# Kernel tuning notes

Hardware: AMD Instinct MI355X
Metric: run time of the kernel (lower is better)

Reference implementation:

```python
import math
import jax, jax.numpy as jnp
import numpy as np

IMG = 1024.0
B = 16
# (h, w, stride, anchor_size) per FPN level
LEVELS = [(256, 256, 4, 32), (128, 128, 8, 64), (64, 64, 16, 128), (32, 32, 32, 256), (16, 16, 64, 512)]
A = 3  # anchors per location (ratios 0.5, 1, 2)
PRE_NMS = 1000   # per level
POST_NMS = 1000
NMS_THRES = 0.7
MIN_SIZE = 1.0
NEG = -1e9
BBOX_CLIP = math.log(1000.0 / 16.0)  # torchvision BoxCoder clamp


def _make_anchors():
    ratios = np.array([0.5, 1.0, 2.0], np.float32)
    hr = np.sqrt(ratios)
    wr = 1.0 / hr
    out = []
    for (h, w, stride, size) in LEVELS:
        ws, hs = size * wr, size * hr
        base = np.stack([-ws / 2, -hs / 2, ws / 2, hs / 2], axis=1)  # [A,4]
        sx = np.arange(w, dtype=np.float32) * stride
        sy = np.arange(h, dtype=np.float32) * stride
        gy, gx = np.meshgrid(sy, sx, indexing='ij')
        shifts = np.stack([gx.ravel(), gy.ravel(), gx.ravel(), gy.ravel()], axis=1)  # [h*w,4]
        out.append((shifts[:, None, :] + base[None, :, :]).reshape(-1, 4))
    return np.concatenate(out, axis=0).astype(np.float32)  # [261888,4]


def setup_inputs() -> dict:
    key = jax.random.key(0)
    ks = jax.random.split(key, 10)
    inp = {}
    for i, (h, w, _, _) in enumerate(LEVELS):
        inp[f'cls{i}'] = jax.random.normal(ks[i], (B, A, h, w), jnp.float32)
        inp[f'box{i}'] = jax.random.normal(ks[5 + i], (B, 4 * A, h, w), jnp.float32) * 0.1
    inp['anchors'] = jnp.asarray(_make_anchors())
    return inp


def _process(x, C):
    # view(B,-1,C,h,w) -> permute(0,3,4,1,2) -> reshape(B,-1,C)
    b, ac, h, w = x.shape
    a = ac // C
    return x.reshape(b, a, C, h, w).transpose(0, 3, 4, 1, 2).reshape(b, -1, C)


def _decode(deltas, anchors):
    # BoxCoder.decode with weights (1,1,1,1)
    aw = anchors[..., 2] - anchors[..., 0]
    ah = anchors[..., 3] - anchors[..., 1]
    ax = anchors[..., 0] + 0.5 * aw
    ay = anchors[..., 1] + 0.5 * ah
    dx, dy = deltas[..., 0], deltas[..., 1]
    dw = jnp.minimum(deltas[..., 2], BBOX_CLIP)
    dh = jnp.minimum(deltas[..., 3], BBOX_CLIP)
    px = dx * aw + ax
    py = dy * ah + ay
    pw = jnp.exp(dw) * aw
    ph = jnp.exp(dh) * ah
    return jnp.stack([px - 0.5 * pw, py - 0.5 * ph, px + 0.5 * pw, py + 0.5 * ph], axis=-1)


def _iou_one_vs_all(box, boxes):
    lt = jnp.maximum(box[:2], boxes[:, :2])
    rb = jnp.minimum(box[2:], boxes[:, 2:])
    wh = jnp.clip(rb - lt, 0.0)
    inter = wh[:, 0] * wh[:, 1]
    a1 = (box[2] - box[0]) * (box[3] - box[1])
    a2 = (boxes[:, 2] - boxes[:, 0]) * (boxes[:, 3] - boxes[:, 1])
    return inter / (a1 + a2 - inter + 1e-9)


def _nms(boxes, scores):
    # iterative hard NMS, fixed POST_NMS iterations (jit-friendly)
    def step(sc, _):
        j = jnp.argmax(sc)
        s = sc[j]
        b = boxes[j]
        valid = s > NEG * 0.5
        iou = _iou_one_vs_all(b, boxes)
        sc = jnp.where(iou > NMS_THRES, NEG, sc)
        sc = sc.at[j].set(NEG)
        return sc, (jnp.where(valid, b, 0.0), jnp.where(valid, s, NEG))
    _, (kb, ks) = jax.lax.scan(step, scores, None, length=POST_NMS)
    return kb, ks


def _forward(clsL, boxL, anchors):
    obj = jnp.concatenate([_process(c, 1) for c in clsL], axis=1)[..., 0]   # [B, N]
    deltas = jnp.concatenate([_process(b, 4) for b in boxL], axis=1)        # [B, N, 4]
    proposals = _decode(jax.lax.stop_gradient(deltas), anchors[None])       # [B, N, 4]

    # per-level pre-NMS top-k on objectness logits
    idx_list, off = [], 0
    for (h, w, _, _) in LEVELS:
        n_l = A * h * w
        k = min(PRE_NMS, n_l)
        _, idx = jax.lax.top_k(obj[:, off:off + n_l], k)
        idx_list.append(idx + off)
        off += n_l
    idx = jnp.concatenate(idx_list, axis=1)                                 # [B, K]

    logits = jnp.take_along_axis(obj, idx, axis=1)
    boxes = jnp.take_along_axis(proposals, idx[..., None], axis=1)
    boxes = jnp.clip(boxes, 0.0, IMG)                                       # clip to image
    probs = jax.nn.sigmoid(logits)
    ws = boxes[..., 2] - boxes[..., 0]
    hs = boxes[..., 3] - boxes[..., 1]
    keep = (ws >= MIN_SIZE) & (hs >= MIN_SIZE)                              # remove small boxes
    probs = jnp.where(keep, probs, NEG)

    kb, ks = jax.vmap(_nms)(boxes, probs)                                   # [B,POST_NMS,4],[B,POST_NMS]
    return kb, ks


def reference(cls0, cls1, cls2, cls3, cls4, box0, box1, box2, box3, box4, anchors):
    return _forward([cls0, cls1, cls2, cls3, cls4], [box0, box1, box2, box3, box4], anchors)
```

## Files before the change

kernel.cpp:

```cpp
#include <hip/hip_runtime.h>
#include <stdint.h>


#define NBATCH 16
#define KSUM 4768
#define NEGF -1e9f
#define CAP 4096
#define CAPB 4096
#define PFX 1664
#define PW 26
typedef unsigned long long u64;
typedef unsigned int u32;

struct Ptrs {
  const float* cls[5];
  const float* box[5];
  const float* anc;
};

__constant__ int c_hw[5]      = {65536, 16384, 4096, 1024, 256};
__constant__ int c_lghw[5]    = {16, 14, 12, 10, 8};
__constant__ int c_K[5]       = {1000, 1000, 1000, 1000, 768};
__constant__ int c_levNOff[5] = {0, 196608, 245760, 258048, 261120};
__constant__ int c_selOff[5]  = {0, 1000, 2000, 3000, 4000};
__constant__ u32 c_guess[4] = {0xC0133333u, 0xBFE00000u, 0xBF8CCCCDu, 0xBE4CCCCDu};

__device__ __forceinline__ u32 monokey(float f) {
  u32 u = __float_as_uint(f);
  return (u & 0x80000000u) ? ~u : (u | 0x80000000u);
}
__device__ __forceinline__ float inv_monokey(u32 k) {
  return __uint_as_float((k & 0x80000000u) ? (k ^ 0x80000000u) : ~k);
}
__device__ __forceinline__ u64 lanemask_lt(int lane) {
  return lane ? ((~0ULL) >> (64 - lane)) : 0ULL;
}

__device__ float sigmoid_xla(float x) {
  #pragma clang fp contract(off)
  float h = 0.5f * x;
  float hc = fminf(fmaxf(h, -7.90531110763549805f), 7.90531110763549805f);
  float x2 = hc * hc;
  float p = -2.76076847742355e-16f;
  p = p * x2 + 2.00018790482477e-13f;
  p = p * x2 + -8.60467152213735e-11f;
  p = p * x2 + 5.12229709037114e-08f;
  p = p * x2 + 1.48572235717979e-05f;
  p = p * x2 + 6.37261928875436e-04f;
  p = p * x2 + 4.89352455891786e-03f;
  p = hc * p;
  float q = 1.19825839466702e-06f;
  q = q * x2 + 1.18534705686654e-04f;
  q = q * x2 + 2.26843463243900e-03f;
  q = q * x2 + 4.89352518554385e-03f;
  float t = (fabsf(h) < 0.0004f) ? h : (p / q);
  return 0.5f + 0.5f * t;
}

__device__ void decode_box(float4 anc, float dx, float dy, float dw, float dh,
                           float& x0, float& y0, float& x1, float& y1, bool& keep) {
  #pragma clang fp contract(off)
  float aw = anc.z - anc.x;
  float ah = anc.w - anc.y;
  float ax = anc.x + 0.5f * aw;
  float ay = anc.y + 0.5f * ah;
  float dwc = fminf(dw, 4.135166556742356f);
  float dhc = fminf(dh, 4.135166556742356f);
  float px = dx * aw + ax;
  float py = dy * ah + ay;
  float pw = expf(dwc) * aw;
  float ph = expf(dhc) * ah;
  x0 = px - 0.5f * pw;
  y0 = py - 0.5f * ph;
  x1 = px + 0.5f * pw;
  y1 = py + 0.5f * ph;
  x0 = fminf(fmaxf(x0, 0.0f), 1024.0f);
  y0 = fminf(fmaxf(y0, 0.0f), 1024.0f);
  x1 = fminf(fmaxf(x1, 0.0f), 1024.0f);
  y1 = fminf(fmaxf(y1, 0.0f), 1024.0f);
  keep = ((x1 - x0) >= 1.0f) && ((y1 - y0) >= 1.0f);
}

__device__ __forceinline__ bool iou_gt(float4 a, float aa, float4 b, float ba) {
  #pragma clang fp contract(off)
  float w = fmaxf(fminf(a.z, b.z) - fmaxf(a.x, b.x), 0.0f);
  float h = fmaxf(fminf(a.w, b.w) - fmaxf(a.y, b.y), 0.0f);
  float inter = w * h;
  float denom = aa + ba - inter + 1e-9f;
  if (inter <= 0.65f * denom) return false;
  return (inter / denom) > 0.7f;
}

__device__ __forceinline__ bool pair_supp(float4 a, float aa, float4 b2, float ba) {
  #pragma clang fp contract(off)
  float w = fmaxf(fminf(a.z, b2.z) - fmaxf(a.x, b2.x), 0.0f);
  float h = fmaxf(fminf(a.w, b2.w) - fmaxf(a.y, b2.y), 0.0f);
  float inter = w * h;
  float denom = aa + ba - inter + 1e-9f;
  bool p65 = inter > 0.65f * denom;
  bool p75 = inter >= 0.75f * denom;
  bool band = p65 && !p75;
  bool supp = p75;
  if (__ballot(band) != 0ULL) {
    if (band) supp = (inter / denom) > 0.7f;
  }
  return supp;
}

__global__ __launch_bounds__(1024) void k_capture(Ptrs p, u64* __restrict__ gCand,
                                                  u32* __restrict__ gCntBlk) {
  const int blk = (int)blockIdx.x;
  const int b = blk / 12, sub = blk % 12;
  int l, s, S;
  if (sub < 8)       { l = 0; s = sub;     S = 8; }
  else if (sub < 10) { l = 1; s = sub - 8; S = 2; }
  else if (sub == 10){ l = 2; s = 0;       S = 1; }
  else               { l = 3; s = 0;       S = 1; }
  const int hw = c_hw[l], lghw = c_lghw[l];
  const int n4 = (3 * hw) >> 2;
  const int per = n4 / S;
  const int tid = threadIdx.x, lane = tid & 63;
  const float4* base4 = (const float4*)(p.cls[l] + (size_t)b * (size_t)(3 * hw)) + (size_t)s * per;
  const int pe0 = 4 * s * per;
  const u32 gk = c_guess[l];

  __shared__ __align__(16) u64 lc[CAPB];
  __shared__ u32 lcnt;
  if (tid == 0) lcnt = 0u;
  __syncthreads();

  for (int i = tid; i < per; i += 1024) {
    float4 v = base4[i];
    float fv[4] = {v.x, v.y, v.z, v.w};
    #pragma unroll
    for (int c = 0; c < 4; ++c) {
      u32 mk = monokey(fv[c]);
      bool cc = (mk >= gk);
      u64 cb = __ballot(cc);
      if (cb) {
        if (cc) {
          int pe = pe0 + 4 * i + c;
          int a = pe >> lghw, cell = pe & (hw - 1);
          u32 nloc = (u32)(cell * 3 + a);
          int leader = __builtin_ctzll(cb);
          u32 wcnt = (u32)__popcll(cb);
          u32 bs;
          if (lane == leader) bs = atomicAdd(&lcnt, wcnt);
          bs = __shfl(bs, leader);
          u32 u = bs + (u32)__popcll(cb & lanemask_lt(lane));
          if (u < CAPB) lc[u] = (((u64)mk) << 32) | nloc;
        }
      }
    }
  }
  __syncthreads();
  const u32 cnt = lcnt;
  const u32 wn = cnt < CAPB ? cnt : CAPB;
  u64* myCand = gCand + (size_t)blk * CAPB;
  for (u32 i = tid; i < wn; i += 1024) myCand[i] = lc[i];
  if (tid == 0) gCntBlk[blk] = cnt;
}

__device__ __forceinline__ void find_thresh(const u32* histF, int nb, u32 K,
                                            u32 cAbove, u32* wsum, u32* wsuf,
                                            u32* shOut, int tid) {
  const int lane = tid & 63, w = tid >> 6;
  u32 h0, h1;
  if (nb == 2048) {
    int b0 = 2 * tid, b1 = b0 + 1;
    h0 = histF[b0] + histF[2048 + b0];
    h1 = histF[b1] + histF[2048 + b1];
  } else {
    h0 = histF[tid] + histF[2048 + tid];
    h1 = 0u;
  }
  u32 x = h0 + h1;
  #pragma unroll
  for (int off = 1; off < 64; off <<= 1) {
    u32 v = __shfl_down(x, off);
    if (lane + off < 64) x += v;
  }
  if (lane == 0) wsum[w] = x;
  __syncthreads();
  if (tid == 0) {
    u32 acc = 0;
    wsuf[16] = 0u;
    for (int q = 15; q >= 0; --q) { acc += wsum[q]; wsuf[q] = acc; }
  }
  __syncthreads();
  u32 SUF0 = x + wsuf[w + 1];
  if (cAbove + SUF0 >= K && cAbove + SUF0 - h0 < K) {
    shOut[0] = (nb == 2048) ? (u32)(2 * tid) : (u32)tid;
    shOut[1] = cAbove + SUF0 - h0;
  }
  if (nb == 2048) {
    u32 SUF1 = SUF0 - h0;
    if (cAbove + SUF1 >= K && cAbove + SUF1 - h1 < K) {
      shOut[0] = (u32)(2 * tid + 1);
      shOut[1] = cAbove + SUF1 - h1;
    }
  }
  __syncthreads();
}

__global__ __launch_bounds__(1024) void k_sel2(Ptrs p, const u64* __restrict__ gCand,
                                               const u32* __restrict__ gCntBlk,
                                               u64* __restrict__ keysC,
                                               u32* __restrict__ cntOut,
                                               float4* __restrict__ boxesWs) {
  const int l = (int)(blockIdx.x % 5);
  const int b = (int)(blockIdx.x / 5);
  const int hw = c_hw[l], lghw = c_lghw[l];
  const int n = 3 * hw, K = c_K[l];
  const int tid = threadIdx.x, lane = tid & 63;

  __shared__ u32 histF[4096];
  __shared__ __align__(16) u64 slots[1024];
  __shared__ __align__(16) u64 cand[CAP];
  __shared__ u32 tieN[1024];
  __shared__ u32 sh[4];
  __shared__ u32 wsum[16], wsuf[17];
  __shared__ u32 subc[8], suboff[9], subBad;

  slots[tid] = 0ULL;
  u32* hc = &histF[((tid >> 6) & 1) * 2048];

  if (K >= n) {
    const float* base = p.cls[l] + (size_t)b * (size_t)n;
    if (tid < n) {
      u32 mk = monokey(base[tid]);
      int a = tid >> lghw, cell = tid & (hw - 1);
      u32 nloc = (u32)(cell * 3 + a);
      slots[tid] = (((u64)mk) << 32) | (0xFFFFFFFFu - nloc);
    }
    __syncthreads();
  } else {
    int subbase, S;
    if (l == 0)      { subbase = 0;  S = 8; }
    else if (l == 1) { subbase = 8;  S = 2; }
    else if (l == 2) { subbase = 10; S = 1; }
    else             { subbase = 11; S = 1; }
    if (tid < (u32)S) subc[tid] = gCntBlk[b * 12 + subbase + tid];
    __syncthreads();
    if (tid == 0) {
      u32 acc = 0, bad = 0;
      for (int t = 0; t < S; ++t) {
        suboff[t] = acc;
        if (subc[t] > CAPB) bad = 1u;
        acc += subc[t];
      }
      suboff[S] = acc;
      subBad = bad;
    }
    __syncthreads();
    const u32 nC = suboff[S];
    u32 threshKey;
    if (!subBad && nC >= (u32)K && nC <= CAP) {
      for (int t = 0; t < S; ++t) {
        const u64* src = gCand + (size_t)(b * 12 + subbase + t) * CAPB;
        u32 c0 = suboff[t], cN = subc[t];
        for (u32 i = tid; i < cN; i += 1024) cand[c0 + i] = src[i];
      }
      for (int i = tid; i < 4096; i += 1024) histF[i] = 0u;
      __syncthreads();
      for (int i = tid; i < (int)nC; i += 1024)
        atomicAdd(&hc[(u32)(cand[i] >> 32) >> 21], 1u);
      __syncthreads();
      find_thresh(histF, 2048, (u32)K, 0u, wsum, wsuf, sh, tid);
      const u32 b0 = sh[0];
      const u32 cA0 = sh[1];
      __syncthreads();
      for (int i = tid; i < 4096; i += 1024) histF[i] = 0u;
      __syncthreads();
      for (int i = tid; i < (int)nC; i += 1024) {
        u32 mk = (u32)(cand[i] >> 32);
        if ((mk >> 21) == b0) atomicAdd(&hc[(mk >> 10) & 0x7FFu], 1u);
      }
      __syncthreads();
      find_thresh(histF, 2048, (u32)K, cA0, wsum, wsuf, sh, tid);
      const u32 b1 = sh[0];
      const u32 cA1 = sh[1];
      const u32 prefix22 = (b0 << 11) | b1;
      __syncthreads();
      for (int i = tid; i < 4096; i += 1024) histF[i] = 0u;
      __syncthreads();
      for (int i = tid; i < (int)nC; i += 1024) {
        u32 mk = (u32)(cand[i] >> 32);
        if ((mk >> 10) == prefix22) atomicAdd(&hc[mk & 0x3FFu], 1u);
      }
      __syncthreads();
      find_thresh(histF, 1024, (u32)K, cA1, wsum, wsuf, sh, tid);
      threshKey = (prefix22 << 10) | sh[0];
      if (tid == 0) { sh[2] = 0u; sh[3] = 0u; }
      __syncthreads();
      for (int i = tid; i < (int)nC; i += 1024) {
        u64 e = cand[i];
        u32 mk = (u32)(e >> 32);
        u32 nloc = (u32)(e & 0xFFFFFFFFull);
        bool gt = (mk > threshKey);
        u64 gb = __ballot(gt);
        if (gt) {
          int leader = __builtin_ctzll(gb);
          u32 wcnt = (u32)__popcll(gb);
          u32 bs;
          if (lane == leader) bs = atomicAdd(&sh[2], wcnt);
          bs = __shfl(bs, leader);
          u32 s2 = bs + (u32)__popcll(gb & lanemask_lt(lane));
          slots[s2] = (((u64)mk) << 32) | (0xFFFFFFFFu - nloc);
        } else if (mk == threshKey) {
          u32 tt = atomicAdd(&sh[3], 1u);
          if (tt < 1024u) tieN[tt] = nloc;
        }
      }
      __syncthreads();
    } else {
      const float* base = p.cls[l] + (size_t)b * (size_t)n;
      const float4* base4 = (const float4*)base;
      const int n4 = n >> 2;
      u32 prefix = 0, cAbove = 0;
      for (int pass = 0; pass < 3; ++pass) {
        for (int i = tid; i < 4096; i += 1024) histF[i] = 0u;
        __syncthreads();
        for (int i = tid; i < n4; i += 1024) {
          float4 v = base4[i];
          float fv[4] = {v.x, v.y, v.z, v.w};
          #pragma unroll
          for (int c = 0; c < 4; ++c) {
            u32 mk = monokey(fv[c]);
            if (pass == 0) atomicAdd(&hc[mk >> 21], 1u);
            else if (pass == 1) { if ((mk >> 21) == prefix) atomicAdd(&hc[(mk >> 10) & 0x7FFu], 1u); }
            else { if ((mk >> 10) == prefix) atomicAdd(&hc[mk & 0x3FFu], 1u); }
          }
        }
        __syncthreads();
        find_thresh(histF, (pass == 2) ? 1024 : 2048, (u32)K, cAbove, wsum, wsuf, sh, tid);
        u32 t = sh[0];
        cAbove = sh[1];
        prefix = (pass == 0) ? t : ((prefix << ((pass == 2) ? 10 : 11)) | t);
        __syncthreads();
      }
      threshKey = prefix;
      if (tid == 0) { sh[2] = 0u; sh[3] = 0u; }
      __syncthreads();
      for (int i = tid; i < n4; i += 1024) {
        float4 v = base4[i];
        float fv[4] = {v.x, v.y, v.z, v.w};
        #pragma unroll
        for (int c = 0; c < 4; ++c) {
          u32 mk = monokey(fv[c]);
          if (mk >= threshKey) {
            int pe = 4 * i + c;
            int a = pe >> lghw, cell = pe & (hw - 1);
            u32 nloc = (u32)(cell * 3 + a);
            if (mk > threshKey) {
              u32 s2 = atomicAdd(&sh[2], 1u);
              slots[s2] = (((u64)mk) << 32) | (0xFFFFFFFFu - nloc);
            } else {
              u32 tt = atomicAdd(&sh[3], 1u);
              if (tt < 1024u) tieN[tt] = nloc;
            }
          }
        }
      }
      __syncthreads();
    }
    if (tid == 0) {
      int cnt = (int)sh[2];
      int need = K - cnt;
      int tc = (int)sh[3];
      if (tc > 1024) tc = 1024;
      for (int s2 = 0; s2 < need; ++s2) {
        u32 best = 0xFFFFFFFFu;
        int bj = -1;
        for (int i2 = 0; i2 < tc; ++i2) {
          u32 v = tieN[i2];
          if (v < best) { best = v; bj = i2; }
        }
        if (bj < 0) break;
        tieN[bj] = 0xFFFFFFFFu;
        slots[cnt + s2] = (((u64)threshKey) << 32) | (0xFFFFFFFFu - best);
      }
    }
    __syncthreads();
  }

  u64 v = slots[tid];
  for (int kk = 2; kk <= 1024; kk <<= 1) {
    for (int j = kk >> 1; j > 0; j >>= 1) {
      u64 pv;
      if (j >= 64) {
        __syncthreads();
        slots[tid] = v;
        __syncthreads();
        pv = slots[tid ^ j];
      } else {
        pv = __shfl_xor(v, j);
      }
      bool takeMax = (((tid & kk) == 0) == ((tid & j) == 0));
      v = takeMax ? ((pv > v) ? pv : v) : ((pv < v) ? pv : v);
    }
  }

  const float4* anc4 = (const float4*)p.anc;
  const float* bxbase = p.box[l];
  const int levN = c_levNOff[l], selO = c_selOff[l];
  bool keepf = false;
  u64 outKey = 0ULL;
  if (tid < K && v != 0ULL) {
    u32 mk = (u32)(v >> 32);
    u32 nloc = 0xFFFFFFFFu - (u32)(v & 0xFFFFFFFFull);
    float logit = inv_monokey(mk);
    int cell = (int)(nloc / 3u);
    int a = (int)(nloc - 3u * (u32)cell);
    const float* dptr = bxbase + (((size_t)(b * 12 + a * 4)) << lghw) + (size_t)cell;
    float dx = dptr[0];
    float dy = dptr[(size_t)hw];
    float dw = dptr[(size_t)2 * (size_t)hw];
    float dh = dptr[(size_t)3 * (size_t)hw];
    float4 anc = anc4[levN + (int)nloc];
    float x0, y0, x1, y1;
    bool keep;
    decode_box(anc, dx, dy, dw, dh, x0, y0, x1, y1, keep);
    int pos = selO + tid;
    boxesWs[(size_t)b * KSUM + (size_t)pos] = make_float4(x0, y0, x1, y1);
    if (keep) {
      float prob = sigmoid_xla(logit);
      keepf = true;
      outKey = (((u64)__float_as_uint(prob)) << 32) | (0xFFFFFFFFu - (u32)pos);
    }
  }
  u64 bal = __ballot(keepf);
  if (lane == 0) wsum[tid >> 6] = (u32)__popcll(bal);
  __syncthreads();
  if (tid < 16) {
    u32 xx = wsum[tid], orig = xx;
    #pragma unroll
    for (int off = 1; off < 16; off <<= 1) {
      u32 vv = __shfl_up(xx, off);
      if (tid >= off) xx += vv;
    }
    wsuf[tid] = xx - orig;
    if (tid == 15) cntOut[b * 5 + l] = xx;
  }
  __syncthreads();
  if (keepf) {
    u32 cidx = wsuf[tid >> 6] + (u32)__popcll(bal & lanemask_lt(lane));
    keysC[((size_t)(b * 5 + l)) * 1000 + cidx] = outKey;
  }
}

__global__ __launch_bounds__(1024) void k_merge(u64* __restrict__ keysC,
                                                const u32* __restrict__ cnt,
                                                float4* __restrict__ boxesWs,
                                                u32* __restrict__ nOut) {
  const int b = blockIdx.x;
  const int tid = threadIdx.x;
  __shared__ u64 keys[5000];
  __shared__ __align__(16) float4 boxes[KSUM];
  __shared__ u32 scnt[5];
  if (tid < 5) scnt[tid] = cnt[b * 5 + tid];
  __syncthreads();
  const int N = (int)(scnt[0] + scnt[1] + scnt[2] + scnt[3] + scnt[4]);
  for (int i = tid; i < 5000; i += 1024) {
    int l = i / 1000, ii = i - l * 1000;
    keys[i] = (ii < (int)scnt[l]) ? keysC[((size_t)(b * 5 + l)) * 1000 + ii] : 0ULL;
  }
  for (int i = tid; i < KSUM; i += 1024) boxes[i] = boxesWs[(size_t)b * KSUM + i];
  __syncthreads();
  #pragma unroll
  for (int q = 0; q < 5; ++q) {
    int s = tid + q * 1024;
    if (s < 5000) {
      int l = s / 1000, ii = s - l * 1000;
      if (ii < (int)scnt[l]) {
        u64 e = keys[s];
        int rank = ii;
        #pragma unroll
        for (int l2 = 0; l2 < 5; ++l2) {
          if (l2 == l) continue;
          int base2 = l2 * 1000;
          int lo = 0, hi = (int)scnt[l2];
          while (lo < hi) {
            int mid = (lo + hi) >> 1;
            if (keys[base2 + mid] > e) lo = mid + 1; else hi = mid;
          }
          rank += lo;
        }
        u32 pos = 0xFFFFFFFFu - (u32)(e & 0xFFFFFFFFull);
        keysC[(size_t)b * 5000 + rank] = e;
        boxesWs[(size_t)b * KSUM + rank] = boxes[pos];
      }
    }
  }
  if (tid == 0) nOut[b] = (u32)N;
}

__global__ __launch_bounds__(1024) void k_mask(const float4* __restrict__ boxesWs,
                                               const u32* __restrict__ nOut,
                                               u64* __restrict__ mat) {
  const int blk = (int)blockIdx.x;
  const int b = blk / 169;
  const int rc = blk - b * 169;
  const int ts = rc / 13, tt = rc - ts * 13;
  const int tid = threadIdx.x;
  u64* matB = mat + (size_t)b * (PW * PFX);
  const int src0 = ts << 7, tgt0 = tt << 7;
  if (ts > tt) {
    if (tid < 256) {
      int s2 = tid & 127, wsel = tid >> 7;
      matB[(size_t)(2 * tt + wsel) * PFX + (size_t)(src0 + s2)] = 0ULL;
    }
    return;
  }
  const int N = (int)nOut[b];
  const int P1 = N < PFX ? N : PFX;
  const float4* mb = boxesWs + (size_t)b * KSUM;

  __shared__ __align__(16) float4 bxS[128];
  __shared__ __align__(16) float4 bxT[128];
  __shared__ float arS[128], arT[128];
  __shared__ u64 slab[256];

  if (tid < 128) {
    int i = src0 + tid;
    float4 v = (i < P1) ? mb[i] : make_float4(0.f, 0.f, 0.f, 0.f);
    bxS[tid] = v;
    {
      #pragma clang fp contract(off)
      arS[tid] = (v.z - v.x) * (v.w - v.y);
    }
  } else if (tid < 256) {
    int j = tgt0 + (tid - 128);
    float4 v = (j < P1) ? mb[j] : make_float4(0.f, 0.f, 0.f, 0.f);
    bxT[tid - 128] = v;
    {
      #pragma clang fp contract(off)
      arT[tid - 128] = (v.z - v.x) * (v.w - v.y);
    }
  }
  __syncthreads();

  const int s = tid >> 3;
  const int slc = tid & 7;
  const float4 my = bxS[s];
  const float myA = arS[s];
  const bool diag = (ts == tt);
  u64 p0 = 0ULL, p1 = 0ULL;
  #pragma unroll
  for (int k = 0; k < 8; ++k) {
    int t = slc + (k << 3);
    bool sp = pair_supp(my, myA, bxT[t], arT[t]);
    sp = sp && (!diag || (s < t));
    p0 |= ((u64)(sp ? 1u : 0u)) << t;
  }
  #pragma unroll
  for (int k = 8; k < 16; ++k) {
    int t = slc + (k << 3);
    bool sp = pair_supp(my, myA, bxT[t], arT[t]);
    sp = sp && (!diag || (s < t));
    p1 |= ((u64)(sp ? 1u : 0u)) << (t - 64);
  }
  #pragma unroll
  for (int off = 1; off < 8; off <<= 1) {
    p0 |= __shfl_xor(p0, off);
    p1 |= __shfl_xor(p1, off);
  }
  if (slc == 0) { slab[s * 2] = p0; slab[s * 2 + 1] = p1; }
  __syncthreads();
  if (tid < 256) {
    int s2 = tid & 127, wsel = tid >> 7;
    matB[(size_t)(2 * tt + wsel) * PFX + (size_t)(src0 + s2)] = slab[s2 * 2 + wsel];
  }
}

__global__ __launch_bounds__(1024) void k_nms(const u64* __restrict__ keysC,
                                              const float4* __restrict__ boxesWs,
                                              const u32* __restrict__ nOut,
                                              const u64* __restrict__ mat,
                                              float* __restrict__ out) {
  const int b = blockIdx.x;
  const int tid = threadIdx.x;
  __shared__ u64 Uw[PW], Kw[PW], remK[PW], ukS[PW], supA[PW], newKw[PW];
  __shared__ u32 wbase[PW + 1];
  __shared__ int mS, doneS;
  __shared__ __align__(16) float4 keptBox[1000];
  __shared__ float keptArea[1000];
  __shared__ __align__(16) float4 chunkBox[128];
  __shared__ float chunkArea[128];
  __shared__ float chunkProb[128];
  __shared__ u32 chunkAlive[128];
  __shared__ u64 suppBy[256];
  __shared__ u64 sAB[2];

  const int N = (int)nOut[b];
  const int P1 = N < PFX ? N : PFX;
  const u64* mk = keysC + (size_t)b * 5000;
  const float4* mb = boxesWs + (size_t)b * KSUM;
  const u64* matC = mat + (size_t)b * (PW * PFX);

  if (tid < PW) {
    int lo = tid << 6;
    int nn = P1 - lo;
    Uw[tid] = (nn >= 64) ? ~0ULL : (nn > 0 ? ((1ULL << nn) - 1ULL) : 0ULL);
    Kw[tid] = 0ULL;
    remK[tid] = 0ULL;
  }
  __syncthreads();

  const int w = tid >> 5;
  const int sub = tid & 31;
  const u64* col = (w < PW) ? (matC + (size_t)w * PFX) : matC;

  for (int round = 0; round < PFX; ++round) {
    if (tid < PW) ukS[tid] = Uw[tid] | Kw[tid];
    __syncthreads();
    {
      u64 acc = 0ULL;
      if (w < PW) {
        int j0 = sub * 52;
        #pragma unroll 4
        for (int jj = 0; jj < 52; ++jj) {
          int j = j0 + jj;
          u64 g = ukS[j >> 6];
          u64 val = col[j];
          acc |= (((g >> (j & 63)) & 1ULL) ? val : 0ULL);
        }
        #pragma unroll
        for (int off = 16; off; off >>= 1) acc |= __shfl_xor(acc, off);
        if (sub == 0) supA[w] = acc;
      }
    }
    __syncthreads();
    if (tid < PW) newKw[tid] = Uw[tid] & ~supA[tid];
    __syncthreads();
    {
      u64 acc = 0ULL;
      if (w < PW) {
        int j0 = sub * 52;
        #pragma unroll 4
        for (int jj = 0; jj < 52; ++jj) {
          int j = j0 + jj;
          u64 g = newKw[j >> 6];
          u64 val = col[j];
          acc |= (((g >> (j & 63)) & 1ULL) ? val : 0ULL);
        }
        #pragma unroll
        for (int off = 16; off; off >>= 1) acc |= __shfl_xor(acc, off);
        if (sub == 0) remK[w] |= acc;
      }
    }
    __syncthreads();
    if (tid < PW) {
      u64 u = Uw[tid], nk = newKw[tid];
      u64 nr = (u & ~nk) & remK[tid];
      Uw[tid] = u & ~nk & ~nr;
      Kw[tid] |= nk;
    }
    __syncthreads();
    if (tid == 0) {
      int d = 1;
      for (int w2 = 0; w2 < PW; ++w2)
        if (Uw[w2]) { d = 0; break; }
      doneS = d;
    }
    __syncthreads();
    if (doneS) break;
  }

  if (tid == 0) {
    u32 acc = 0;
    for (int w2 = 0; w2 < PW; ++w2) {
      wbase[w2] = acc;
      acc += (u32)__popcll(Kw[w2]);
    }
    wbase[PW] = acc;
    mS = (acc < 1000u) ? (int)acc : 1000;
  }
  __syncthreads();
  int m = mS;

  for (int idx = tid; idx < P1; idx += 1024) {
    u64 kw = Kw[idx >> 6];
    int bit = idx & 63;
    if ((kw >> bit) & 1ULL) {
      int g = (int)wbase[idx >> 6] + __popcll(kw & ((1ULL << bit) - 1ULL));
      if (g < 1000) {
        float4 bxv = mb[idx];
        float pr = __uint_as_float((u32)(mk[idx] >> 32));
        float arv;
        {
          #pragma clang fp contract(off)
          arv = (bxv.z - bxv.x) * (bxv.w - bxv.y);
        }
        keptBox[g] = bxv;
        keptArea[g] = arv;
        ((float4*)out)[b * 1000 + g] = bxv;
        out[64000 + b * 1000 + g] = pr;
      }
    }
  }
  __syncthreads();

  for (int cs = PFX; cs < N && m < 1000; cs += 128) {
    if (tid < 128) {
      int idx = cs + tid;
      float4 bxv = make_float4(0.f, 0.f, 0.f, 0.f);
      float arv = 0.f, pr = 0.f;
      u32 alive = 0u;
      if (idx < N) {
        bxv = mb[idx];
        pr = __uint_as_float((u32)(mk[idx] >> 32));
        {
          #pragma clang fp contract(off)
          arv = (bxv.z - bxv.x) * (bxv.w - bxv.y);
        }
        alive = 1u;
      }
      chunkBox[tid] = bxv;
      chunkArea[tid] = arv;
      chunkProb[tid] = pr;
      chunkAlive[tid] = alive;
    }
    if (tid >= 128 && tid < 384) suppBy[tid - 128] = 0ULL;
    __syncthreads();

    {
      int i0 = tid & 127, sl = tid >> 7;
      float4 my = chunkBox[i0];
      float myA = chunkArea[i0];
      bool supp = false;
      #pragma unroll 4
      for (int i = sl; i < m; i += 8) {
        float ka = keptArea[i];
        float4 kb = keptBox[i];
        if (fminf(ka, myA) > 0.699f * fmaxf(ka, myA))
          supp = supp | iou_gt(kb, ka, my, myA);
      }
      if (supp) chunkAlive[i0] = 0u;
    }
    for (int pI = tid; pI < 16384; pI += 1024) {
      int i = pI >> 7, j = pI & 127;
      if (j < i) {
        float aj = chunkArea[j], ai = chunkArea[i];
        if (fminf(aj, ai) > 0.699f * fmaxf(aj, ai)) {
          if (iou_gt(chunkBox[j], aj, chunkBox[i], ai))
            atomicOr(&suppBy[i * 2 + (j >> 6)], 1ULL << (j & 63));
        }
      }
    }
    __syncthreads();

    if (tid < 64) {
      bool aliveLo = chunkAlive[tid] != 0u;
      bool aliveHi = chunkAlive[64 + tid] != 0u;
      u64 sLL = suppBy[tid * 2];
      u64 sHL = suppBy[(64 + tid) * 2];
      u64 sHH = suppBy[(64 + tid) * 2 + 1];
      u64 uLo = sLL;
      #pragma unroll
      for (int off = 1; off < 64; off <<= 1) uLo |= __shfl_xor(uLo, off);
      u64 rem = uLo;
      while (rem) {
        int k = __builtin_ctzll(rem);
        rem &= rem - 1ULL;
        u64 A = __ballot(aliveLo);
        if (((A >> k) & 1ULL) && ((sLL >> k) & 1ULL)) aliveLo = false;
      }
      u64 A0 = __ballot(aliveLo);
      if (sHL & A0) aliveHi = false;
      u64 uHi = sHH;
      #pragma unroll
      for (int off = 1; off < 64; off <<= 1) uHi |= __shfl_xor(uHi, off);
      rem = uHi;
      while (rem) {
        int k = __builtin_ctzll(rem);
        rem &= rem - 1ULL;
        u64 A = __ballot(aliveHi);
        if (((A >> k) & 1ULL) && ((sHH >> k) & 1ULL)) aliveHi = false;
      }
      u64 A1 = __ballot(aliveHi);
      if (tid == 0) { sAB[0] = A0; sAB[1] = A1; }
    }
    __syncthreads();

    u64 A0 = sAB[0], A1 = sAB[1];
    int total = __popcll(A0) + __popcll(A1);
    if (tid < 128) {
      bool kept = (tid < 64) ? ((A0 >> tid) & 1ULL) : ((A1 >> (tid - 64)) & 1ULL);
      if (kept) {
        int rank = (tid < 64)
                       ? __popcll(A0 & ((1ULL << tid) - 1ULL))
                       : (__popcll(A0) + __popcll(A1 & ((1ULL << (tid - 64)) - 1ULL)));
        int g = m + rank;
        if (g < 1000) {
          float4 cb = chunkBox[tid];
          keptBox[g] = cb;
          keptArea[g] = chunkArea[tid];
          ((float4*)out)[b * 1000 + g] = cb;
          out[64000 + b * 1000 + g] = chunkProb[tid];
        }
      }
    }
    m += total;
    if (m > 1000) m = 1000;
    __syncthreads();
  }

  for (int g = m + tid; g < 1000; g += 1024) {
    ((float4*)out)[b * 1000 + g] = make_float4(0.f, 0.f, 0.f, 0.f);
    out[64000 + b * 1000 + g] = NEGF;
  }
}

extern "C" void kernel_launch(void* const* d_in, const int* in_sizes, int n_in,
                              void* d_out, int out_size, void* d_ws, size_t ws_size,
                              hipStream_t stream) {
  bool interleaved = (in_sizes[1] == 16 * 12 * 256 * 256);
  Ptrs p;
  for (int l = 0; l < 5; ++l) {
    p.cls[l] = (const float*)d_in[interleaved ? (2 * l) : l];
    p.box[l] = (const float*)d_in[interleaved ? (2 * l + 1) : (5 + l)];
  }
  p.anc = (const float*)d_in[10];

  u64* keysC = (u64*)d_ws;
  u32* cntW = (u32*)((char*)d_ws + 640000);
  u32* nOut = cntW + 80;
  float4* boxesWs = (float4*)((char*)d_ws + 640512);
  u32* gCntBlk = (u32*)((char*)d_ws + 1861120);
  u64* gCand = (u64*)((char*)d_ws + 1862144);
  u64* mat = gCand;

  k_capture<<<dim3(NBATCH * 12), dim3(1024), 0, stream>>>(p, gCand, gCntBlk);
  k_sel2<<<dim3(NBATCH * 5), dim3(1024), 0, stream>>>(p, gCand, gCntBlk, keysC, cntW, boxesWs);
  k_merge<<<dim3(NBATCH), dim3(1024), 0, stream>>>(keysC, cntW, boxesWs, nOut);
  k_mask<<<dim3(NBATCH * 169), dim3(1024), 0, stream>>>(boxesWs, nOut, mat);
  k_nms<<<dim3(NBATCH), dim3(1024), 0, stream>>>(keysC, boxesWs, nOut, mat, (float*)d_out);
}
```

Baseline: 116.1 us.

## Compact undecided and newly-kept bitmasks into index lists for sparse NMS matrix OR

```diff
diff --git a/kernel.cpp b/kernel.cpp
--- a/kernel.cpp
+++ b/kernel.cpp
@@ -11,6 +11,7 @@
 #define PW 26
 typedef unsigned long long u64;
 typedef unsigned int u32;
+typedef unsigned short u16;
 
 struct Ptrs {
   const float* cls[5];
@@ -580,9 +581,13 @@
                                               float* __restrict__ out) {
   const int b = blockIdx.x;
   const int tid = threadIdx.x;
-  __shared__ u64 Uw[PW], Kw[PW], remK[PW], ukS[PW], supA[PW], newKw[PW];
+  __shared__ u64 Uw[PW], Kw[PW], remK[PW], supA[PW], newKw[PW];
+  __shared__ u16 ulist[PFX];
+  __shared__ u16 klist[PFX];
+  __shared__ u32 ubase[PW], kbase[PW];
+  __shared__ int nUS, nKS;
   __shared__ u32 wbase[PW + 1];
-  __shared__ int mS, doneS;
+  __shared__ int mS;
   __shared__ __align__(16) float4 keptBox[1000];
   __shared__ float keptArea[1000];
   __shared__ __align__(16) float4 chunkBox[128];
@@ -612,38 +617,55 @@
   const u64* col = (w < PW) ? (matC + (size_t)w * PFX) : matC;
 
   for (int round = 0; round < PFX; ++round) {
-    if (tid < PW) ukS[tid] = Uw[tid] | Kw[tid];
+    if (tid == 0) {
+      u32 acc = 0;
+      for (int w2 = 0; w2 < PW; ++w2) { ubase[w2] = acc; acc += (u32)__popcll(Uw[w2]); }
+      nUS = (int)acc;
+    }
+    __syncthreads();
+    const int nU = nUS;
+    if (nU == 0) break;
+    for (int idx = tid; idx < P1; idx += 1024) {
+      u64 uw = Uw[idx >> 6];
+      int bit = idx & 63;
+      if ((uw >> bit) & 1ULL) {
+        int pos = (int)ubase[idx >> 6] + __popcll(uw & ((1ULL << bit) - 1ULL));
+        ulist[pos] = (u16)idx;
+      }
+    }
     __syncthreads();
     {
       u64 acc = 0ULL;
       if (w < PW) {
-        int j0 = sub * 52;
-        #pragma unroll 4
-        for (int jj = 0; jj < 52; ++jj) {
-          int j = j0 + jj;
-          u64 g = ukS[j >> 6];
-          u64 val = col[j];
-          acc |= (((g >> (j & 63)) & 1ULL) ? val : 0ULL);
-        }
+        for (int li = sub; li < nU; li += 32) acc |= col[(int)ulist[li]];
         #pragma unroll
         for (int off = 16; off; off >>= 1) acc |= __shfl_xor(acc, off);
-        if (sub == 0) supA[w] = acc;
+        if (sub == 0) supA[w] = acc | remK[w];
       }
     }
     __syncthreads();
     if (tid < PW) newKw[tid] = Uw[tid] & ~supA[tid];
+    __syncthreads();
+    if (tid == 0) {
+      u32 acc = 0;
+      for (int w2 = 0; w2 < PW; ++w2) { kbase[w2] = acc; acc += (u32)__popcll(newKw[w2]); }
+      nKS = (int)acc;
+    }
+    __syncthreads();
+    const int nK = nKS;
+    for (int idx = tid; idx < P1; idx += 1024) {
+      u64 kw2 = newKw[idx >> 6];
+      int bit = idx & 63;
+      if ((kw2 >> bit) & 1ULL) {
+        int pos = (int)kbase[idx >> 6] + __popcll(kw2 & ((1ULL << bit) - 1ULL));
+        klist[pos] = (u16)idx;
+      }
+    }
     __syncthreads();
     {
       u64 acc = 0ULL;
       if (w < PW) {
-        int j0 = sub * 52;
-        #pragma unroll 4
-        for (int jj = 0; jj < 52; ++jj) {
-          int j = j0 + jj;
-          u64 g = newKw[j >> 6];
-          u64 val = col[j];
-          acc |= (((g >> (j & 63)) & 1ULL) ? val : 0ULL);
-        }
+        for (int li = sub; li < nK; li += 32) acc |= col[(int)klist[li]];
         #pragma unroll
         for (int off = 16; off; off >>= 1) acc |= __shfl_xor(acc, off);
         if (sub == 0) remK[w] |= acc;
@@ -657,14 +679,6 @@
       Kw[tid] |= nk;
     }
     __syncthreads();
-    if (tid == 0) {
-      int d = 1;
-      for (int w2 = 0; w2 < PW; ++w2)
-        if (Uw[w2]) { d = 0; break; }
-      doneS = d;
-    }
-    __syncthreads();
-    if (doneS) break;
   }
 
   if (tid == 0) {
```

Result: no change. 115.2 us (-0.8%).
